# Kernel optimization log

Hardware: AMD Instinct MI355X
Metric: run time of the kernel (lower is better)

## Reference

```python
import jax, jax.numpy as jnp
import numpy as np

N = 100000   # nodes
E = 1600000  # edges (node pairs)
D = 64       # msg_feature_len
H = 128      # hidden width of gate/message MLPs


def setup_inputs() -> dict:
    key = jax.random.key(0)
    ks = jax.random.split(key, 10)
    s = 0.05
    return {
        "node_weights": jax.random.uniform(ks[0], (N, 1), dtype=jnp.float32),
        "node_prev_features": jax.random.normal(ks[1], (N, D), dtype=jnp.float32),
        "self_idx": jax.random.randint(ks[2], (E,), 0, N),
        "neighbor_idx": jax.random.randint(ks[3], (E,), 0, N),
        "gw1": jax.random.normal(ks[4], (2 * D, H), dtype=jnp.float32) * s,
        "gb1": jnp.zeros((H,), jnp.float32),
        "gw2": jax.random.normal(ks[5], (H, 1), dtype=jnp.float32) * s,
        "gb2": jnp.zeros((1,), jnp.float32),
        "mw1": jax.random.normal(ks[6], (2 * D, H), dtype=jnp.float32) * s,
        "mb1": jnp.zeros((H,), jnp.float32),
        "mw2": jax.random.normal(ks[7], (H, D), dtype=jnp.float32) * s,
        "mb2": jnp.zeros((D,), jnp.float32),
        "pow_p": jax.random.normal(ks[8], (1,), dtype=jnp.float32),
    }


def reference(node_weights, node_prev_features, self_idx, neighbor_idx,
              gw1, gb1, gw2, gb2, mw1, mb1, mw2, mb2, pow_p):
    # gather + concat: message [E, 2D]
    msg = jnp.concatenate(
        [node_prev_features[self_idx], node_prev_features[neighbor_idx]], axis=1)
    w = node_weights[neighbor_idx]  # [E, 1]

    # gate MLP (Linear -> ReLU -> Linear): [E, 1]
    gate = jax.nn.relu(msg @ gw1 + gb1) @ gw2 + gb2
    # segment-softmax over edges grouped by self_idx, weighted by w**pow
    gmax = jax.ops.segment_max(gate, self_idx, num_segments=N)  # [N, 1]
    gate = (w ** pow_p) * jnp.exp(gate - gmax[self_idx])
    gsum = jax.ops.segment_sum(gate, self_idx, num_segments=N)  # [N, 1]
    gate = gate / (gsum[self_idx] + 1e-10)

    # message MLP: [E, D]
    x = jax.nn.relu(msg @ mw1 + mb1) @ mw2 + mb2

    # weighted scatter-sum back to nodes; single head -> mean is identity
    node_update = jax.ops.segment_sum(gate * x, self_idx, num_segments=N)
    return node_update + node_prev_features
```

## Files before the change

kernel.cpp:

```cpp
#include <hip/hip_runtime.h>
#include <hip/hip_bf16.h>

typedef __bf16 bf16x8 __attribute__((ext_vector_type(8)));
typedef float f32x4 __attribute__((ext_vector_type(4)));
typedef float f32x2 __attribute__((ext_vector_type(2)));

#define WIN 64
#define TILE 112
#define CHUNK 7
#define LSTR 136
#define SCAN_BLK 1024
#define SENT 0x7f7f7f7f

static __device__ __forceinline__ void dec8(unsigned x, unsigned y, float* o) {
    f32x2 a = __builtin_amdgcn_cvt_pk_f32_fp8(x, false);
    f32x2 b = __builtin_amdgcn_cvt_pk_f32_fp8(x, true);
    f32x2 c = __builtin_amdgcn_cvt_pk_f32_fp8(y, false);
    f32x2 d = __builtin_amdgcn_cvt_pk_f32_fp8(y, true);
    o[0] = a[0]; o[1] = a[1]; o[2] = b[0]; o[3] = b[1];
    o[4] = c[0]; o[5] = c[1]; o[6] = d[0]; o[7] = d[1];
}

__global__ void k_wconv(const float* __restrict__ gw1, const float* __restrict__ mw1,
                        const float* __restrict__ mw2,
                        __bf16* __restrict__ Bt, __bf16* __restrict__ mw2t,
                        int* __restrict__ hist, int* __restrict__ s_lo,
                        int* __restrict__ s_hi, int N, int NB)
{
    int i = blockIdx.x * 256 + threadIdx.x;
    if (i < 32768) {
        int c = i >> 6, k = i & 63;
        float v;
        if (c < 128)      v = gw1[k * 128 + c];
        else if (c < 256) v = gw1[(64 + k) * 128 + (c - 128)];
        else if (c < 384) v = mw1[k * 128 + (c - 256)];
        else              v = mw1[(64 + k) * 128 + (c - 384)];
        Bt[i] = (__bf16)v;
    } else if (i < 40960) {
        int j = i - 32768;
        int c = j >> 7, k = j & 127;
        mw2t[j] = (__bf16)mw2[k * 64 + c];
    }
    if (i < N) hist[i] = 0;
    if (i < NB) { s_lo[i] = SENT; s_hi[i] = 0; }
}

__global__ void __launch_bounds__(256, 4)
k_tab(const float* __restrict__ feat, const __bf16* __restrict__ Bt,
      const float* __restrict__ gb1, const float* __restrict__ mb1,
      const int* __restrict__ selfi, int* __restrict__ hist,
      unsigned char* __restrict__ Tp, unsigned char* __restrict__ Tq, int N, int E)
{
    __shared__ unsigned char ldsT[2][16][256];

    for (int e = blockIdx.x * 256 + threadIdx.x; e < E; e += gridDim.x * 256)
        atomicAdd(&hist[selfi[e]], 1);

    const int tid = threadIdx.x;
    const int lane = tid & 63, wv = tid >> 6;
    const int la = lane & 15, kg = lane >> 4;
    const int r0 = blockIdx.x * 16;
    if (r0 >= N) return;

    bf16x8 a[2];
    #pragma unroll
    for (int kk = 0; kk < 2; ++kk) {
        const int rr = min(r0 + la, N - 1);
        const float* src = feat + (size_t)rr * 64 + kk * 32 + kg * 8;
        f32x4 f0 = *reinterpret_cast<const f32x4*>(src);
        f32x4 f1 = *reinterpret_cast<const f32x4*>(src + 4);
        #pragma unroll
        for (int j = 0; j < 4; ++j) { a[kk][j] = (__bf16)f0[j]; a[kk][4 + j] = (__bf16)f1[j]; }
    }
    #pragma unroll
    for (int j = 0; j < 8; ++j) {
        const int c = wv * 128 + j * 16 + la;
        float bias = 0.f;
        if (c < 128) bias = gb1[c];
        else if (c >= 256 && c < 384) bias = mb1[c - 256];
        f32x4 acc = {bias, bias, bias, bias};
        #pragma unroll
        for (int kk = 0; kk < 2; ++kk) {
            bf16x8 bb = *reinterpret_cast<const bf16x8*>(Bt + (size_t)c * 64 + kk * 32 + kg * 8);
            acc = __builtin_amdgcn_mfma_f32_16x16x32_bf16(a[kk], bb, acc, 0, 0, 0);
        }
        int tbl, boff;
        if (c < 128)      { tbl = 0; boff = ((c) >> 3) * 16 + (c & 7); }
        else if (c < 256) { const int q = c - 128; tbl = 1; boff = (q >> 3) * 16 + (q & 7); }
        else if (c < 384) { const int q = c - 256; tbl = 0; boff = (q >> 3) * 16 + 8 + (q & 7); }
        else              { const int q = c - 384; tbl = 1; boff = (q >> 3) * 16 + 8 + (q & 7); }
        #pragma unroll
        for (int i = 0; i < 4; ++i) {
            const int pk = __builtin_amdgcn_cvt_pk_fp8_f32(acc[i], acc[i], 0, false);
            ldsT[tbl][kg * 4 + i][boff] = (unsigned char)(pk & 0xff);
        }
    }
    __syncthreads();
    {
        const int row = tid >> 4, v4 = tid & 15;
        if (r0 + row < N) {
            const uint4* s0p = reinterpret_cast<const uint4*>(&ldsT[0][row][0]);
            const uint4* s1p = reinterpret_cast<const uint4*>(&ldsT[1][row][0]);
            reinterpret_cast<uint4*>(Tp + (size_t)(r0 + row) * 256)[v4] = s0p[v4];
            reinterpret_cast<uint4*>(Tq + (size_t)(r0 + row) * 256)[v4] = s1p[v4];
        }
    }
}

__global__ void k_scan1(const int* __restrict__ hist, int* __restrict__ incl,
                        int* __restrict__ bsum, int N)
{
    __shared__ int sd[SCAN_BLK];
    int i = blockIdx.x * SCAN_BLK + threadIdx.x;
    int v = (i < N) ? hist[i] : 0;
    sd[threadIdx.x] = v;
    __syncthreads();
    for (int off = 1; off < SCAN_BLK; off <<= 1) {
        int t = (threadIdx.x >= off) ? sd[threadIdx.x - off] : 0;
        __syncthreads();
        sd[threadIdx.x] += t;
        __syncthreads();
    }
    if (i < N) incl[i] = sd[threadIdx.x];
    if (threadIdx.x == SCAN_BLK - 1) bsum[blockIdx.x] = sd[SCAN_BLK - 1];
}

__global__ void k_scanb(const int* __restrict__ bsum, int* __restrict__ boff, int nb)
{
    __shared__ int sd[256];
    const int t = threadIdx.x;
    int v = (t < nb) ? bsum[t] : 0;
    sd[t] = v;
    __syncthreads();
    for (int off = 1; off < 256; off <<= 1) {
        int u = (t >= off) ? sd[t - off] : 0;
        __syncthreads();
        sd[t] += u;
        __syncthreads();
    }
    if (t < nb) boff[t] = sd[t] - v;
}

__global__ void k_scan23(const int* __restrict__ incl, const int* __restrict__ hist,
                         const int* __restrict__ boff,
                         int* __restrict__ cursor, int* __restrict__ starts,
                         int* __restrict__ s_lo, int* __restrict__ s_hi,
                         float* __restrict__ lpw, const float* __restrict__ nodew,
                         const float* __restrict__ powp,
                         const float* __restrict__ prev, float* __restrict__ out,
                         int N, int E)
{
    int i = blockIdx.x * SCAN_BLK + threadIdx.x;
    if (i >= N) return;
    const int h = hist[i];
    const int v = incl[i] - h + boff[blockIdx.x];
    cursor[i] = v;
    starts[i] = v;
    lpw[i] = powp[0] * __logf(nodew[i]);
    if (h > 0) {
        const int b = v / WIN;
        atomicMin(&s_lo[b], i);
        atomicMax(&s_hi[b], i + 1);
    } else {
        const float* ps = prev + (size_t)i * 64;
        float* po = out + (size_t)i * 64;
        for (int k = 0; k < 64; ++k) po[k] = ps[k];
    }
}

__global__ void k_scatter(const int* __restrict__ selfi, const int* __restrict__ nbri,
                          int* __restrict__ cursor, int* __restrict__ nbr_p, int E)
{
    int e = blockIdx.x * 256 + threadIdx.x;
    if (e >= E) return;
    int s = selfi[e];
    int pos = atomicAdd(&cursor[s], 1);
    nbr_p[pos] = nbri[e];
}

__global__ void __launch_bounds__(256, 5)
k_fused(const unsigned char* __restrict__ Tp, const unsigned char* __restrict__ Tq,
        const int* __restrict__ nbr_p, const int* __restrict__ starts,
        const int* __restrict__ s_lo, const int* __restrict__ s_hi,
        const float* __restrict__ lpw,
        const float* __restrict__ gw2, const float* __restrict__ gb2,
        const __bf16* __restrict__ mw2t, const float* __restrict__ mb2,
        const float* __restrict__ prev, float* __restrict__ out,
        int N, int E)
{
    __shared__ __align__(16) __bf16 hlds[TILE][LSTR];
    __shared__ float logit_s[TILE];
    __shared__ float ginv_s[WIN];
    __shared__ int st_s[WIN + 1];

    const int b = blockIdx.x;
    const int s0 = s_lo[b];
    if (s0 == SENT) return;
    const int s1 = s_hi[b];
    const int nseg = s1 - s0;
    const int e0 = starts[s0];
    const int e1 = (s1 < N) ? starts[s1] : E;
    int ne = e1 - e0;
    if (ne > TILE) ne = TILE;

    const int tid = threadIdx.x;
    for (int j = tid; j <= nseg; j += 256)
        st_s[j] = (j < nseg) ? starts[s0 + j] : e1;
    __syncthreads();

    const int lane = tid & 63, wv = tid >> 6;
    const int g16 = tid >> 4, il = tid & 15;

    {
        const float b2v = gb2[0];
        float w2f[8];
        {
            f32x4 wa = *reinterpret_cast<const f32x4*>(gw2 + il * 8);
            f32x4 wb = *reinterpret_cast<const f32x4*>(gw2 + il * 8 + 4);
            w2f[0] = wa[0]; w2f[1] = wa[1]; w2f[2] = wa[2]; w2f[3] = wa[3];
            w2f[4] = wb[0]; w2f[5] = wb[1]; w2f[6] = wb[2]; w2f[7] = wb[3];
        }
        const int ck = (ne + 15) >> 4;
        const int rb = g16 * ck;
        const int re = min(rb + ck, ne);
        const int m = re - rb;
        if (m > 0) {
            uint4 qv[CHUNK];
            float lpv[CHUNK];
            #pragma unroll
            for (int j = 0; j < CHUNK; ++j) {
                const int rc = (j < m) ? (rb + j) : (re - 1);
                const int nn = nbr_p[e0 + rc];
                qv[j] = *reinterpret_cast<const uint4*>(Tq + (size_t)nn * 256 + il * 16);
                lpv[j] = lpw[nn];
            }
            int cur;
            {
                int lo = 0, hi = nseg - 1;
                while (lo < hi) {
                    const int mid = (lo + hi + 1) >> 1;
                    if (st_s[mid] <= e0 + rb) lo = mid; else hi = mid - 1;
                }
                cur = lo;
            }
            int curlim = st_s[cur + 1];
            float pgf[8], pmf[8];
            {
                const uint4 tpv = *reinterpret_cast<const uint4*>(Tp + (size_t)(s0 + cur) * 256 + il * 16);
                dec8(tpv.x, tpv.y, pgf);
                dec8(tpv.z, tpv.w, pmf);
            }
            #pragma unroll
            for (int j = 0; j < CHUNK; ++j) {
                if (j < m) {
                    const int r = rb + j;
                    if (e0 + r >= curlim) {
                        do { ++cur; curlim = st_s[cur + 1]; } while (e0 + r >= curlim);
                        const uint4 tpv = *reinterpret_cast<const uint4*>(Tp + (size_t)(s0 + cur) * 256 + il * 16);
                        dec8(tpv.x, tpv.y, pgf);
                        dec8(tpv.z, tpv.w, pmf);
                    }
                    float qgv[8], qmv[8];
                    dec8(qv[j].x, qv[j].y, qgv);
                    dec8(qv[j].z, qv[j].w, qmv);
                    float lg = 0.f;
                    bf16x8 hv;
                    #pragma unroll
                    for (int q = 0; q < 8; ++q) {
                        lg = fmaf(fmaxf(pgf[q] + qgv[q], 0.f), w2f[q], lg);
                        hv[q] = (__bf16)fmaxf(pmf[q] + qmv[q], 0.f);
                    }
                    *reinterpret_cast<bf16x8*>(&hlds[r][il * 8]) = hv;
                    #pragma unroll
                    for (int sh = 1; sh < 16; sh <<= 1)
                        lg += __shfl_xor(lg, sh, 16);
                    if (il == 0) logit_s[r] = lg + b2v + lpv[j];
                }
            }
        }
    }
    __syncthreads();

    const int la = lane & 15, kg = lane >> 4;
    const int row0[2] = {wv * 16, 64 + wv * 16};
    const bool lv[2] = {row0[0] < ne, (wv < 3) && (row0[1] < ne)};

    f32x4 c2[2][4] = {};
    #pragma unroll
    for (int kk = 0; kk < 4; ++kk) {
        const int kbase = kk * 32 + kg * 8;
        bf16x8 a[2];
        #pragma unroll
        for (int m = 0; m < 2; ++m)
            if (lv[m]) a[m] = *reinterpret_cast<const bf16x8*>(&hlds[row0[m] + la][kbase]);
        #pragma unroll
        for (int n = 0; n < 4; ++n) {
            bf16x8 bb = *reinterpret_cast<const bf16x8*>(mw2t + (size_t)(n * 16 + la) * 128 + kbase);
            #pragma unroll
            for (int m = 0; m < 2; ++m)
                if (lv[m]) c2[m][n] = __builtin_amdgcn_mfma_f32_16x16x32_bf16(a[m], bb, c2[m][n], 0, 0, 0);
        }
    }

    for (int j = g16; j < nseg; j += 16) {
        int a0 = st_s[j] - e0;
        int a1 = st_s[j + 1] - e0;
        if (a1 > ne) a1 = ne;
        float mx = -3.4e38f;
        for (int idx = a0 + il; idx < a1; idx += 16)
            mx = fmaxf(mx, logit_s[idx]);
        #pragma unroll
        for (int sh = 1; sh < 16; sh <<= 1)
            mx = fmaxf(mx, __shfl_xor(mx, sh, 16));
        float sum = 0.f;
        for (int idx = a0 + il; idx < a1; idx += 16) {
            const float g = __expf(logit_s[idx] - mx);
            logit_s[idx] = g;
            sum += g;
        }
        #pragma unroll
        for (int sh = 1; sh < 16; sh <<= 1)
            sum += __shfl_xor(sum, sh, 16);
        if (il == 0) ginv_s[j] = 1.f / (sum + 1e-10f);
    }
    __syncthreads();

    float (*xb)[68] = reinterpret_cast<float(*)[68]>(&hlds[0][0]);
    #pragma unroll
    for (int m = 0; m < 2; ++m) {
        if (!lv[m]) continue;
        float cf[4];
        #pragma unroll
        for (int i = 0; i < 4; ++i) {
            const int row = row0[m] + kg * 4 + i;
            cf[i] = (row < ne) ? logit_s[row] : 0.f;
        }
        #pragma unroll
        for (int n = 0; n < 4; ++n) {
            const float b2v = mb2[n * 16 + la];
            #pragma unroll
            for (int i = 0; i < 4; ++i)
                xb[row0[m] + kg * 4 + i][n * 16 + la] = cf[i] * (c2[m][n][i] + b2v);
        }
    }
    __syncthreads();

    for (int j = wv; j < nseg; j += 4) {
        int a0 = st_s[j] - e0;
        int a1 = st_s[j + 1] - e0;
        if (a1 > ne) a1 = ne;
        if (a1 <= a0) continue;
        float sum = 0.f;
        for (int r = a0; r < a1; ++r) sum += xb[r][lane];
        const float gi = ginv_s[j];
        const size_t o = (size_t)(s0 + j) * 64 + lane;
        out[o] = prev[o] + sum * gi;
    }
}

extern "C" void kernel_launch(void* const* d_in, const int* in_sizes, int n_in,
                              void* d_out, int out_size, void* d_ws, size_t ws_size,
                              hipStream_t stream)
{
    const float* node_w = (const float*)d_in[0];
    const float* prev   = (const float*)d_in[1];
    const int*   selfi  = (const int*)d_in[2];
    const int*   nbri   = (const int*)d_in[3];
    const float* gw1 = (const float*)d_in[4];
    const float* gb1 = (const float*)d_in[5];
    const float* gw2 = (const float*)d_in[6];
    const float* gb2 = (const float*)d_in[7];
    const float* mw1 = (const float*)d_in[8];
    const float* mb1 = (const float*)d_in[9];
    const float* mw2 = (const float*)d_in[10];
    const float* mb2 = (const float*)d_in[11];
    const float* powp = (const float*)d_in[12];
    const int N = in_sizes[0];
    const int E = in_sizes[2];
    float* out = (float*)d_out;
    const int NB = (E + WIN - 1) / WIN;

    char* ws = (char*)d_ws;
    size_t off = 0;
    auto alloc = [&](size_t bytes) {
        void* p = ws + off;
        off = (off + bytes + 255) & ~(size_t)255;
        return p;
    };
    unsigned char* Tp    = (unsigned char*)alloc((size_t)N * 256);
    unsigned char* Tq    = (unsigned char*)alloc((size_t)N * 256);
    __bf16* Bt           = (__bf16*)alloc(512 * 64 * 2);
    __bf16* mw2t         = (__bf16*)alloc(64 * 128 * 2);
    int* nbr_p           = (int*)alloc((size_t)E * 4);
    int* hist            = (int*)alloc((size_t)N * 4);
    int* cursor          = (int*)alloc((size_t)N * 4);
    int* starts          = (int*)alloc((size_t)N * 4);
    int* incl            = (int*)alloc((size_t)N * 4);
    float* lpw           = (float*)alloc((size_t)N * 4);
    int* s_lo            = (int*)alloc((size_t)NB * 4);
    int* s_hi            = (int*)alloc((size_t)NB * 4);
    const int nb = (N + SCAN_BLK - 1) / SCAN_BLK;
    int* bsum            = (int*)alloc((size_t)nb * 4);
    int* boff            = (int*)alloc((size_t)nb * 4);

    int initN = N;
    if (initN < 40960) initN = 40960;
    if (initN < NB) initN = NB;
    k_wconv<<<(initN + 255) / 256, 256, 0, stream>>>(gw1, mw1, mw2, Bt, mw2t,
                                                     hist, s_lo, s_hi, N, NB);
    k_tab<<<(N + 15) / 16, 256, 0, stream>>>(prev, Bt, gb1, mb1, selfi, hist, Tp, Tq, N, E);
    k_scan1<<<nb, SCAN_BLK, 0, stream>>>(hist, incl, bsum, N);
    k_scanb<<<1, 256, 0, stream>>>(bsum, boff, nb);
    k_scan23<<<nb, SCAN_BLK, 0, stream>>>(incl, hist, boff, cursor, starts, s_lo, s_hi,
                                          lpw, node_w, powp, prev, out, N, E);
    k_scatter<<<(E + 255) / 256, 256, 0, stream>>>(selfi, nbri, cursor, nbr_p, E);
    k_fused<<<NB, 256, 0, stream>>>(Tp, Tq, nbr_p, starts, s_lo, s_hi, lpw,
                                    gw2, gb2, mw2t, mb2, prev, out, N, E);
}
```

Baseline: 481.7 us.

## Store hidden tile in LDS as fp8, fold block-offset scan into scan23, raise occupancy

Drops the single-block k_scanb launch; each k_scan23 block now sums the preceding block totals itself with a wave reduction. In k_fused, the hidden activations are packed to fp8 in LDS and unpacked to bf16 before the MFMA, and the weighted message tile is stored as bf16 instead of fp32. Together these shrink LDS use so launch bounds can go from 5 to 8 waves per SIMD. The cost is lower precision in the second matmul input and in the per-edge partial sums, plus extra convert instructions and tighter register limits that may cause spills.

Result: slower. 532.7 us (+10.6%).

```diff
diff --git a/kernel.cpp b/kernel.cpp
--- a/kernel.cpp
+++ b/kernel.cpp
@@ -8,7 +8,7 @@
 #define WIN 64
 #define TILE 112
 #define CHUNK 7
-#define LSTR 136
+#define HSTR 136
 #define SCAN_BLK 1024
 #define SENT 0x7f7f7f7f
 
@@ -125,24 +125,8 @@
     if (threadIdx.x == SCAN_BLK - 1) bsum[blockIdx.x] = sd[SCAN_BLK - 1];
 }
 
-__global__ void k_scanb(const int* __restrict__ bsum, int* __restrict__ boff, int nb)
-{
-    __shared__ int sd[256];
-    const int t = threadIdx.x;
-    int v = (t < nb) ? bsum[t] : 0;
-    sd[t] = v;
-    __syncthreads();
-    for (int off = 1; off < 256; off <<= 1) {
-        int u = (t >= off) ? sd[t - off] : 0;
-        __syncthreads();
-        sd[t] += u;
-        __syncthreads();
-    }
-    if (t < nb) boff[t] = sd[t] - v;
-}
-
 __global__ void k_scan23(const int* __restrict__ incl, const int* __restrict__ hist,
-                         const int* __restrict__ boff,
+                         const int* __restrict__ bsum,
                          int* __restrict__ cursor, int* __restrict__ starts,
                          int* __restrict__ s_lo, int* __restrict__ s_hi,
                          float* __restrict__ lpw, const float* __restrict__ nodew,
@@ -150,10 +134,19 @@
                          const float* __restrict__ prev, float* __restrict__ out,
                          int N, int E)
 {
+    __shared__ int boff_s;
+    if (threadIdx.x < 64) {
+        int part = 0;
+        for (int j = threadIdx.x; j < (int)blockIdx.x; j += 64) part += bsum[j];
+        #pragma unroll
+        for (int sh = 1; sh < 64; sh <<= 1) part += __shfl_xor(part, sh, 64);
+        if (threadIdx.x == 0) boff_s = part;
+    }
+    __syncthreads();
     int i = blockIdx.x * SCAN_BLK + threadIdx.x;
     if (i >= N) return;
     const int h = hist[i];
-    const int v = incl[i] - h + boff[blockIdx.x];
+    const int v = incl[i] - h + boff_s;
     cursor[i] = v;
     starts[i] = v;
     lpw[i] = powp[0] * __logf(nodew[i]);
@@ -178,7 +171,7 @@
     nbr_p[pos] = nbri[e];
 }
 
-__global__ void __launch_bounds__(256, 5)
+__global__ void __launch_bounds__(256, 8)
 k_fused(const unsigned char* __restrict__ Tp, const unsigned char* __restrict__ Tq,
         const int* __restrict__ nbr_p, const int* __restrict__ starts,
         const int* __restrict__ s_lo, const int* __restrict__ s_hi,
@@ -188,7 +181,7 @@
         const float* __restrict__ prev, float* __restrict__ out,
         int N, int E)
 {
-    __shared__ __align__(16) __bf16 hlds[TILE][LSTR];
+    __shared__ __align__(16) unsigned char hlds8[TILE][HSTR];
     __shared__ float logit_s[TILE];
     __shared__ float ginv_s[WIN];
     __shared__ int st_s[WIN + 1];
@@ -264,13 +257,17 @@
                     dec8(qv[j].x, qv[j].y, qgv);
                     dec8(qv[j].z, qv[j].w, qmv);
                     float lg = 0.f;
-                    bf16x8 hv;
+                    float hm[8];
                     #pragma unroll
                     for (int q = 0; q < 8; ++q) {
                         lg = fmaf(fmaxf(pgf[q] + qgv[q], 0.f), w2f[q], lg);
-                        hv[q] = (__bf16)fmaxf(pmf[q] + qmv[q], 0.f);
+                        hm[q] = fmaxf(pmf[q] + qmv[q], 0.f);
                     }
-                    *reinterpret_cast<bf16x8*>(&hlds[r][il * 8]) = hv;
+                    unsigned d0 = __builtin_amdgcn_cvt_pk_fp8_f32(hm[0], hm[1], 0, false);
+                    d0 = __builtin_amdgcn_cvt_pk_fp8_f32(hm[2], hm[3], d0, true);
+                    unsigned d1 = __builtin_amdgcn_cvt_pk_fp8_f32(hm[4], hm[5], 0, false);
+                    d1 = __builtin_amdgcn_cvt_pk_fp8_f32(hm[6], hm[7], d1, true);
+                    *reinterpret_cast<uint2*>(&hlds8[r][il * 8]) = make_uint2(d0, d1);
                     #pragma unroll
                     for (int sh = 1; sh < 16; sh <<= 1)
                         lg += __shfl_xor(lg, sh, 16);
@@ -288,17 +285,23 @@
     f32x4 c2[2][4] = {};
     #pragma unroll
     for (int kk = 0; kk < 4; ++kk) {
-        const int kbase = kk * 32 + kg * 8;
+        const int kboff = kk * 32 + kg * 8;
         bf16x8 a[2];
         #pragma unroll
-        for (int m = 0; m < 2; ++m)
-            if (lv[m]) a[m] = *reinterpret_cast<const bf16x8*>(&hlds[row0[m] + la][kbase]);
+        for (int m2 = 0; m2 < 2; ++m2)
+            if (lv[m2]) {
+                const uint2 hw = *reinterpret_cast<const uint2*>(&hlds8[row0[m2] + la][kboff]);
+                float t[8];
+                dec8(hw.x, hw.y, t);
+                #pragma unroll
+                for (int q = 0; q < 8; ++q) a[m2][q] = (__bf16)t[q];
+            }
         #pragma unroll
         for (int n = 0; n < 4; ++n) {
-            bf16x8 bb = *reinterpret_cast<const bf16x8*>(mw2t + (size_t)(n * 16 + la) * 128 + kbase);
+            bf16x8 bb = *reinterpret_cast<const bf16x8*>(mw2t + (size_t)(n * 16 + la) * 128 + kboff);
             #pragma unroll
-            for (int m = 0; m < 2; ++m)
-                if (lv[m]) c2[m][n] = __builtin_amdgcn_mfma_f32_16x16x32_bf16(a[m], bb, c2[m][n], 0, 0, 0);
+            for (int m2 = 0; m2 < 2; ++m2)
+                if (lv[m2]) c2[m2][n] = __builtin_amdgcn_mfma_f32_16x16x32_bf16(a[m2], bb, c2[m2][n], 0, 0, 0);
         }
     }
 
@@ -325,22 +328,19 @@
     }
     __syncthreads();
 
-    float (*xb)[68] = reinterpret_cast<float(*)[68]>(&hlds[0][0]);
+    __bf16 (*xb)[68] = reinterpret_cast<__bf16(*)[68]>(&hlds8[0][0]);
     #pragma unroll
-    for (int m = 0; m < 2; ++m) {
-        if (!lv[m]) continue;
-        float cf[4];
-        #pragma unroll
-        for (int i = 0; i < 4; ++i) {
-            const int row = row0[m] + kg * 4 + i;
-            cf[i] = (row < ne) ? logit_s[row] : 0.f;
-        }
+    for (int m2 = 0; m2 < 2; ++m2) {
+        if (!lv[m2]) continue;
         #pragma unroll
         for (int n = 0; n < 4; ++n) {
             const float b2v = mb2[n * 16 + la];
             #pragma unroll
-            for (int i = 0; i < 4; ++i)
-                xb[row0[m] + kg * 4 + i][n * 16 + la] = cf[i] * (c2[m][n][i] + b2v);
+            for (int i = 0; i < 4; ++i) {
+                const int row = row0[m2] + kg * 4 + i;
+                const float v = (row < ne) ? logit_s[row] * (c2[m2][n][i] + b2v) : 0.f;
+                xb[row][n * 16 + la] = (__bf16)v;
+            }
         }
     }
     __syncthreads();
@@ -351,7 +351,7 @@
         if (a1 > ne) a1 = ne;
         if (a1 <= a0) continue;
         float sum = 0.f;
-        for (int r = a0; r < a1; ++r) sum += xb[r][lane];
+        for (int r = a0; r < a1; ++r) sum += (float)xb[r][lane];
         const float gi = ginv_s[j];
         const size_t o = (size_t)(s0 + j) * 64 + lane;
         out[o] = prev[o] + sum * gi;
@@ -401,7 +401,6 @@
     int* s_hi            = (int*)alloc((size_t)NB * 4);
     const int nb = (N + SCAN_BLK - 1) / SCAN_BLK;
     int* bsum            = (int*)alloc((size_t)nb * 4);
-    int* boff            = (int*)alloc((size_t)nb * 4);
 
     int initN = N;
     if (initN < 40960) initN = 40960;
@@ -410,8 +409,7 @@
                                                      hist, s_lo, s_hi, N, NB);
     k_tab<<<(N + 15) / 16, 256, 0, stream>>>(prev, Bt, gb1, mb1, selfi, hist, Tp, Tq, N, E);
     k_scan1<<<nb, SCAN_BLK, 0, stream>>>(hist, incl, bsum, N);
-    k_scanb<<<1, 256, 0, stream>>>(bsum, boff, nb);
-    k_scan23<<<nb, SCAN_BLK, 0, stream>>>(incl, hist, boff, cursor, starts, s_lo, s_hi,
+    k_scan23<<<nb, SCAN_BLK, 0, stream>>>(incl, hist, bsum, cursor, starts, s_lo, s_hi,
                                           lpw, node_w, powp, prev, out, N, E);
     k_scatter<<<(E + 255) / 256, 256, 0, stream>>>(selfi, nbri, cursor, nbr_p, E);
     k_fused<<<NB, 256, 0, stream>>>(Tp, Tq, nbr_p, starts, s_lo, s_hi, lpw,
```
